# Performance work log

Measured on AMD Instinct MI355X. Metric: run time of the kernel, lower is better.

The kernel has to match this reference:

```python
import jax, jax.numpy as jnp
import numpy as np

# Hard-coded model hyperparams (RuntimeParams)
B, L, H, NH, FF, DEPTH = 256, 256, 128, 8, 512, 4
PEAK, NCAT, CVOC, KMAX, NNUM, NDIM, TSLOT = 500000, 8, 50001, 8, 4, 32, 256
SCALE = (H // NH) ** -0.5


def _ln(x, g, b):
    m = x.mean(-1, keepdims=True)
    v = ((x - m) ** 2).mean(-1, keepdims=True)
    return (x - m) / jnp.sqrt(v + 1e-5) * g + b


def _block(x, mask, p):
    ln1_g, ln1_b, qw, qb, ow, ob, w1, b1, w2, b2, ln2_g, ln2_b = p
    b, n, c = x.shape
    src = _ln(x, ln1_g, ln1_b)
    qkv = (src @ qw + qb).reshape(b, n, 3, NH, c // NH).transpose(2, 0, 3, 1, 4)
    q, k, v = qkv[0], qkv[1], qkv[2]  # [b, nh, n, dh]
    dots = jnp.einsum('bhid,bhjd->bhij', q, k) * SCALE
    dots = jnp.where(mask[:, None, None, :], dots, -jnp.inf)
    attn = jax.nn.softmax(dots, axis=-1)
    out = jnp.einsum('bhij,bhjd->bhid', attn, v).transpose(0, 2, 1, 3).reshape(b, n, c)
    x = x + out @ ow + ob
    h = _ln(x, ln2_g, ln2_b)
    h = jax.nn.gelu(h @ w1 + b1, approximate=False) @ w2 + b2
    return x + h


def _encode(cat_vals, cat_lens, num_arr, cat_tables, num_W):
    # Vectorized form of the per-sample _encode_fields python loop:
    # per categorical field: mean of embeddings over the ragged value list
    # per numeric field: bias-free linear projection; then mean over all fields.
    emb = cat_tables[jnp.arange(NCAT)[None, :, None], cat_vals]  # [B,F,K,H]
    pos = (jnp.arange(KMAX)[None, None, :] < cat_lens[:, :, None]).astype(emb.dtype)
    fc = (emb * pos[..., None]).sum(2) / cat_lens[:, :, None].astype(emb.dtype)  # [B,F,H]
    fn = jnp.einsum('bfd,fdh->bfh', num_arr, num_W)  # [B,Fn,H]
    return (fc.sum(1) + fn.sum(1)) / (NCAT + NNUM)  # mean over all fields


def setup_inputs() -> dict:
    key = jax.random.key(0)
    ks = iter(jax.random.split(key, 40))
    nk = lambda: next(ks)
    d = {}
    d['item_seq'] = jax.random.randint(nk(), (B, L), 0, PEAK + 5)
    d['action_seq'] = jax.random.randint(nk(), (B, L), 0, 5)
    d['time_diff'] = jax.random.randint(nk(), (B, L), 0, TSLOT)
    seq_lens = jax.random.randint(nk(), (B,), L // 2, L + 1)
    d['mask'] = jnp.arange(L)[None, :] < seq_lens[:, None]
    for pre in ('u', 'i'):
        vals = jax.random.randint(nk(), (B, NCAT, KMAX), 1, CVOC)
        lens = jax.random.randint(nk(), (B, NCAT), 1, KMAX + 1)
        vals = jnp.where(jnp.arange(KMAX)[None, None, :] < lens[:, :, None], vals, 0)
        d[pre + '_cat_vals'] = vals
        d[pre + '_cat_lens'] = lens
        d[pre + '_num'] = jax.random.normal(nk(), (B, NNUM, NDIM), dtype=jnp.float32)
    s = 0.02
    d['item_table'] = (jax.random.normal(nk(), (PEAK + 5, H), dtype=jnp.float32) * s).at[0].set(0.0)
    d['act_table'] = jax.random.normal(nk(), (5, H), dtype=jnp.float32) * s
    d['time_table'] = jax.random.normal(nk(), (TSLOT, H), dtype=jnp.float32) * s
    d['cat_tables'] = (jax.random.normal(nk(), (NCAT, CVOC, H), dtype=jnp.float32) * s).at[:, 0, :].set(0.0)
    d['num_W'] = jax.random.normal(nk(), (NNUM, NDIM, H), dtype=jnp.float32) * s
    d['global_token'] = jax.random.normal(nk(), (1, 1, H), dtype=jnp.float32)
    d['ln1_g'] = jnp.ones((DEPTH, H)); d['ln1_b'] = jnp.zeros((DEPTH, H))
    d['qkv_w'] = jax.random.normal(nk(), (DEPTH, H, 3 * H), dtype=jnp.float32) * s
    d['qkv_b'] = jnp.zeros((DEPTH, 3 * H))
    d['out_w'] = jax.random.normal(nk(), (DEPTH, H, H), dtype=jnp.float32) * s
    d['out_b'] = jnp.zeros((DEPTH, H))
    d['mlp_w1'] = jax.random.normal(nk(), (DEPTH, H, FF), dtype=jnp.float32) * s
    d['mlp_b1'] = jnp.zeros((DEPTH, FF))
    d['mlp_w2'] = jax.random.normal(nk(), (DEPTH, FF, H), dtype=jnp.float32) * s
    d['mlp_b2'] = jnp.zeros((DEPTH, H))
    d['ln2_g'] = jnp.ones((DEPTH, H)); d['ln2_b'] = jnp.zeros((DEPTH, H))
    d['bott_w'] = jax.random.normal(nk(), (H, H), dtype=jnp.float32) * s
    d['bott_b'] = jnp.zeros((H,))
    d['cls_w'] = jax.random.normal(nk(), (H, 1), dtype=jnp.float32) * s
    d['cls_b'] = jnp.zeros((1,))
    return d


def reference(item_seq, action_seq, time_diff, mask, u_cat_vals, u_cat_lens, u_num,
              i_cat_vals, i_cat_lens, i_num, item_table, act_table, time_table,
              cat_tables, num_W, global_token, ln1_g, ln1_b, qkv_w, qkv_b,
              out_w, out_b, mlp_w1, mlp_b1, mlp_w2, mlp_b2, ln2_g, ln2_b,
              bott_w, bott_b, cls_w, cls_b):
    b = item_seq.shape[0]
    seq_feat = item_table[item_seq] + act_table[action_seq] + time_table[time_diff]  # [B,L,H]
    u = _encode(u_cat_vals, u_cat_lens, u_num, cat_tables, num_W)[:, None, :]
    i = _encode(i_cat_vals, i_cat_lens, i_num, cat_tables, num_W)[:, None, :]
    cls = jnp.broadcast_to(global_token, (b, 1, H))
    x = jnp.concatenate([cls, u, i, seq_feat], axis=1)  # [B, 3+L, H]
    fmask = jnp.concatenate([jnp.ones((b, 3), dtype=bool), mask], axis=1)
    for dd in range(DEPTH):
        p = (ln1_g[dd], ln1_b[dd], qkv_w[dd], qkv_b[dd], out_w[dd], out_b[dd],
             mlp_w1[dd], mlp_b1[dd], mlp_w2[dd], mlp_b2[dd], ln2_g[dd], ln2_b[dd])
        x = _block(x, fmask, p)
    latent = x[:, 0, :]
    logits = (jax.nn.relu(latent @ bott_w + bott_b) @ cls_w + cls_b)[:, 0]
    embed = latent / jnp.maximum(jnp.linalg.norm(latent, axis=-1, keepdims=True), 1e-12)
    return logits, embed
```

## Files before the change

### kernel.cpp

```cpp
#include <hip/hip_runtime.h>
#include <cstdio>

#define BATCH 256
#define SEQL 256
#define NPOS 259
#define TTOK (BATCH*NPOS)
#define HD 128
#define NHEAD 8
#define FF 512
#define DEPTH 4
#define CVOC 50001

typedef unsigned short u16;
typedef unsigned int u32;
typedef __bf16 bf16x8 __attribute__((ext_vector_type(8)));
typedef float f32x4 __attribute__((ext_vector_type(4)));
typedef float f32x16 __attribute__((ext_vector_type(16)));

typedef const __attribute__((address_space(1))) u32 gas_u32;
typedef __attribute__((address_space(3))) u32 las_u32;
#define GLOAD16(gptr, lptr) \
  __builtin_amdgcn_global_load_lds((gas_u32*)(gptr), (las_u32*)(lptr), 16, 0, 0)

#define QSCALE 0.36067376022224085f

__device__ __forceinline__ u16 f2bf(float f) {
  u32 i = __float_as_uint(f);
  u32 r = (i + 0x7FFFu + ((i >> 16) & 1u)) >> 16;
  return (u16)r;
}
__device__ __forceinline__ float bf2f(u16 u) {
  return __uint_as_float(((u32)u) << 16);
}

__global__ void k_transpose_all(const float* __restrict__ qkv_w, const float* __restrict__ out_w,
                                const float* __restrict__ w1, const float* __restrict__ w2,
                                u16* __restrict__ wT) {
  int idx = blockIdx.x * 256 + threadIdx.x;
  const float* in; int K, N, local;
  if (idx < 196608)      { in = qkv_w; K = 128; N = 384; local = idx; }
  else if (idx < 262144) { in = out_w; K = 128; N = 128; local = idx - 196608; }
  else if (idx < 524288) { in = w1;    K = 128; N = 512; local = idx - 262144; }
  else if (idx < 786432) { in = w2;    K = 512; N = 128; local = idx - 524288; }
  else return;
  int k = local % K; int rem = local / K; int n = rem % N; int d = rem / N;
  wT[idx] = f2bf(in[(d * K + k) * N + n]);
}

__global__ __launch_bounds__(128)
void k_build(const int* __restrict__ item_seq, const int* __restrict__ act_seq,
             const int* __restrict__ tdiff,
             const int* __restrict__ ucv, const int* __restrict__ ucl, const float* __restrict__ unum,
             const int* __restrict__ icv, const int* __restrict__ icl, const float* __restrict__ inum,
             const float* __restrict__ item_t, const float* __restrict__ act_t,
             const float* __restrict__ time_t, const float* __restrict__ cat_t,
             const float* __restrict__ numW, const float* __restrict__ gtok,
             const float* __restrict__ g, const float* __restrict__ be,
             u16* __restrict__ x, u16* __restrict__ src) {
  int pos = blockIdx.x, b = blockIdx.y, h = threadIdx.x;
  float v;
  if (pos == 0) {
    v = gtok[h];
  } else if (pos <= 2) {
    const int* cv = (pos == 1) ? ucv : icv;
    const int* cl = (pos == 1) ? ucl : icl;
    const float* nm = (pos == 1) ? unum : inum;
    float acc = 0.f;
    for (int f = 0; f < 8; ++f) {
      float s = 0.f;
      for (int k = 0; k < 8; ++k) {
        int idx = cv[(b * 8 + f) * 8 + k];
        s += cat_t[((size_t)f * CVOC + idx) * HD + h];
      }
      acc += s / (float)cl[b * 8 + f];
    }
    for (int f = 0; f < 4; ++f)
      for (int d = 0; d < 32; ++d)
        acc += nm[(b * 4 + f) * 32 + d] * numW[(f * 32 + d) * HD + h];
    v = acc * (1.f / 12.f);
  } else {
    int l = pos - 3;
    v = item_t[(size_t)item_seq[b * SEQL + l] * HD + h]
      + act_t[(size_t)act_seq[b * SEQL + l] * HD + h]
      + time_t[(size_t)tdiff[b * SEQL + l] * HD + h];
  }
  size_t t = (size_t)b * NPOS + pos;
  x[t * HD + h] = f2bf(v);
  __shared__ float red[2][2];
  float s = v, s2 = v * v;
  #pragma unroll
  for (int o = 32; o; o >>= 1) { s += __shfl_xor(s, o); s2 += __shfl_xor(s2, o); }
  if ((h & 63) == 0) { red[h >> 6][0] = s; red[h >> 6][1] = s2; }
  __syncthreads();
  float S = red[0][0] + red[1][0], S2 = red[0][1] + red[1][1];
  float mean = S * (1.f / HD);
  float rstd = rsqrtf(S2 * (1.f / HD) - mean * mean + 1e-5f);
  src[t * HD + h] = f2bf((v - mean) * rstd * g[h] + be[h]);
}

template <int NCH, int ACT, bool QS>
__global__ __launch_bounds__(256)
void k_gemm_nres(const u16* __restrict__ X, const u16* __restrict__ WT,
                 const float* __restrict__ bias, u16* __restrict__ outp) {
  const int K = 128, N = NCH * 128;
  __shared__ __align__(16) u16 lA[4][32 * 32];
  __shared__ __align__(16) u16 lB[128 * 32];
  const int tid = threadIdx.x;
  const int wave = tid >> 6, lane = tid & 63;
  const int row0 = blockIdx.x * 32;
  const int wr = (wave >> 1) * 16, wc = (wave & 1) * 64;
  const int sr = lane >> 2;
  const int sc = ((lane & 3) ^ ((lane >> 3) & 3)) << 3;
  const int q = lane & 15;
  const int cg = lane >> 4;
  const int rdoff = ((cg ^ ((q >> 1) & 3)) << 3);
  GLOAD16(X + (size_t)(row0 + sr) * K + wave * 32 + sc, &lA[wave][0]);
  GLOAD16(X + (size_t)(row0 + 16 + sr) * K + wave * 32 + sc, &lA[wave][512]);
  const u16* gB0 = WT + (size_t)(wave * 16 + sr) * K + sc;
  const u16* gB1 = WT + (size_t)(64 + wave * 16 + sr) * K + sc;
  u16* lB0 = &lB[wave * 512];
  u16* lB1 = &lB[2048 + wave * 512];
  for (int nc = 0; nc < NCH; ++nc) {
    const size_t nbase = (size_t)nc * 128 * K;
    f32x4 acc[4] = {};
    for (int k0 = 0; k0 < K; k0 += 32) {
      __syncthreads();
      GLOAD16(gB0 + nbase + k0, lB0);
      GLOAD16(gB1 + nbase + k0, lB1);
      __syncthreads();
      const int kt = k0 >> 5;
      bf16x8 af = *(const bf16x8*)&lA[kt][(wr + q) * 32 + rdoff];
      bf16x8 bf[4];
      #pragma unroll
      for (int j = 0; j < 4; ++j)
        bf[j] = *(const bf16x8*)&lB[(wc + j * 16 + q) * 32 + rdoff];
      #pragma unroll
      for (int j = 0; j < 4; ++j)
        acc[j] = __builtin_amdgcn_mfma_f32_16x16x32_bf16(af, bf[j], acc[j], 0, 0, 0);
    }
    const int rg4 = cg * 4;
    const float scl = (QS && nc == 0) ? QSCALE : 1.f;
    #pragma unroll
    for (int j = 0; j < 4; ++j) {
      int col = nc * 128 + wc + j * 16 + q;
      float bv = bias[col];
      #pragma unroll
      for (int jj = 0; jj < 4; ++jj) {
        int row = row0 + wr + rg4 + jj;
        float v = acc[j][jj] + bv;
        if (ACT == 1) v = 0.5f * v * (1.f + erff(v * 0.70710678118654752f));
        if (QS) v *= scl;
        outp[(size_t)row * N + col] = f2bf(v);
      }
    }
  }
}

__global__ __launch_bounds__(256)
void k_gemm_ln(const u16* __restrict__ X, const u16* __restrict__ WT,
               const float* __restrict__ bias, u16* __restrict__ xio,
               const float* __restrict__ g, const float* __restrict__ be,
               u16* __restrict__ srcout, int K) {
  __shared__ __align__(16) u16 lA[32 * 32];
  __shared__ __align__(16) u16 lB[128 * 32];
  __shared__ float part[32][2][2];
  const int tid = threadIdx.x;
  const int wave = tid >> 6, lane = tid & 63;
  const int row0 = blockIdx.x * 32;
  const int wr = (wave >> 1) * 16, wc = (wave & 1) * 64;
  const int whalf = wave & 1;
  const int sr = lane >> 2;
  const int sc = ((lane & 3) ^ ((lane >> 3) & 3)) << 3;
  const u16* gA = X + (size_t)(row0 + (wave & 1) * 16 + sr) * K + sc;
  const u16* gB0 = WT + (size_t)(wave * 16 + sr) * K + sc;
  const u16* gB1 = WT + (size_t)(64 + wave * 16 + sr) * K + sc;
  u16* lA0 = &lA[(wave & 1) * 512];
  u16* lB0 = &lB[wave * 512];
  u16* lB1 = &lB[2048 + wave * 512];
  const int q = lane & 15;
  const int cg = lane >> 4;
  const int rdoff = ((cg ^ ((q >> 1) & 3)) << 3);
  f32x4 acc[4] = {};
  for (int k0 = 0; k0 < K; k0 += 32) {
    __syncthreads();
    if (wave < 2) GLOAD16(gA + k0, lA0);
    GLOAD16(gB0 + k0, lB0);
    GLOAD16(gB1 + k0, lB1);
    __syncthreads();
    bf16x8 af = *(const bf16x8*)&lA[(wr + q) * 32 + rdoff];
    bf16x8 bf[4];
    #pragma unroll
    for (int j = 0; j < 4; ++j)
      bf[j] = *(const bf16x8*)&lB[(wc + j * 16 + q) * 32 + rdoff];
    #pragma unroll
    for (int j = 0; j < 4; ++j)
      acc[j] = __builtin_amdgcn_mfma_f32_16x16x32_bf16(af, bf[j], acc[j], 0, 0, 0);
  }
  const int rg4 = cg * 4;
  float ps[4], ps2[4];
  #pragma unroll
  for (int jj = 0; jj < 4; ++jj) { ps[jj] = 0.f; ps2[jj] = 0.f; }
  #pragma unroll
  for (int j = 0; j < 4; ++j) {
    int col = wc + j * 16 + q;
    float bv = bias[col];
    #pragma unroll
    for (int jj = 0; jj < 4; ++jj) {
      int row = row0 + wr + rg4 + jj;
      float xv = bf2f(xio[(size_t)row * 128 + col]) + acc[j][jj] + bv;
      acc[j][jj] = xv;
      ps[jj] += xv;
      ps2[jj] += xv * xv;
    }
  }
  #pragma unroll
  for (int o = 1; o < 16; o <<= 1) {
    #pragma unroll
    for (int jj = 0; jj < 4; ++jj) {
      ps[jj]  += __shfl_xor(ps[jj], o);
      ps2[jj] += __shfl_xor(ps2[jj], o);
    }
  }
  if (q == 0) {
    #pragma unroll
    for (int jj = 0; jj < 4; ++jj) {
      int rl = wr + rg4 + jj;
      part[rl][whalf][0] = ps[jj];
      part[rl][whalf][1] = ps2[jj];
    }
  }
  __syncthreads();
  #pragma unroll
  for (int jj = 0; jj < 4; ++jj) {
    int rl = wr + rg4 + jj;
    float S  = part[rl][0][0] + part[rl][1][0];
    float S2 = part[rl][0][1] + part[rl][1][1];
    float mean = S * (1.f / 128.f);
    float rstd = rsqrtf(S2 * (1.f / 128.f) - mean * mean + 1e-5f);
    int row = row0 + rl;
    #pragma unroll
    for (int j = 0; j < 4; ++j) {
      int col = wc + j * 16 + q;
      float xv = acc[j][jj];
      xio[(size_t)row * 128 + col] = f2bf(xv);
      srcout[(size_t)row * 128 + col] = f2bf((xv - mean) * rstd * g[col] + be[col]);
    }
  }
}

#define VSTR2 296
__global__ __launch_bounds__(576)
void k_attn(const u16* __restrict__ qkv, const int* __restrict__ mask,
            u16* __restrict__ out) {
  int b = blockIdx.x, h = blockIdx.y;
  __shared__ __align__(16) u16 Klin[9 * 512];
  __shared__ __align__(16) u16 Vt[16 * VSTR2];
  __shared__ int part[4];
  const int tid = threadIdx.x;
  if (tid < 256) {
    int mv = (mask[b * SEQL + tid] != 0) ? 1 : 0;
    #pragma unroll
    for (int o = 32; o; o >>= 1) mv += __shfl_xor(mv, o);
    if ((tid & 63) == 0) part[tid >> 6] = mv;
  }
  {
    int r = tid >> 1, h2 = tid & 1;
    uint4 val = make_uint4(0, 0, 0, 0);
    if (r < NPOS)
      val = *(const uint4*)&qkv[((size_t)(b * NPOS + r)) * 384 + h * 16 + 128 + h2 * 8];
    *(uint4*)&Klin[(r >> 5) * 512 + h2 * 256 + (r & 31) * 8] = val;
  }
  {
    int r = tid >> 1, h2 = tid & 1;
    if (r < 288) {
      u16 tmp[8];
      if (r < NPOS) {
        *(uint4*)tmp = *(const uint4*)&qkv[((size_t)(b * NPOS + r)) * 384 + h * 16 + 256 + h2 * 8];
      } else {
        #pragma unroll
        for (int d = 0; d < 8; ++d) tmp[d] = 0;
      }
      #pragma unroll
      for (int d = 0; d < 8; ++d) Vt[(h2 * 8 + d) * VSTR2 + r] = tmp[d];
    }
  }
  __syncthreads();
  const int nvalid = part[0] + part[1] + part[2] + part[3] + 3;
  const int ktiles = (nvalid + 31) >> 5;
  const int wave = tid >> 6, lane = tid & 63;
  const int q5 = lane & 31, hi = lane >> 5;
  const f32x16 zf = {};
  const int qt = wave;
  int qrow = qt * 32 + q5;
  int qr = (qrow < NPOS) ? qrow : (NPOS - 1);
  bf16x8 qf = *(const bf16x8*)&qkv[((size_t)(b * NPOS + qr)) * 384 + h * 16 + hi * 8];
  float m = -1e30f, l = 0.f;
  f32x16 acc = {};
  for (int kt = 0; kt < ktiles; ++kt) {
    bf16x8 kf = *(const bf16x8*)&Klin[kt * 512 + lane * 8];
    __builtin_amdgcn_s_setprio(1);
    f32x16 s4 = __builtin_amdgcn_mfma_f32_32x32x16_bf16(kf, qf, zf, 0, 0, 0);
    __builtin_amdgcn_s_setprio(0);
    float p[16];
    float tmax = -1e30f;
    if ((kt + 1) * 32 <= nvalid) {
      #pragma unroll
      for (int r = 0; r < 16; ++r) { p[r] = s4[r]; tmax = fmaxf(tmax, s4[r]); }
    } else {
      #pragma unroll
      for (int r = 0; r < 16; ++r) {
        int kr = kt * 32 + (r & 3) + 8 * (r >> 2) + 4 * hi;
        float v = (kr < nvalid) ? s4[r] : -1e30f;
        p[r] = v;
        tmax = fmaxf(tmax, v);
      }
    }
    tmax = fmaxf(tmax, __shfl_xor(tmax, 32));
    bool defer = __all(tmax <= m + 8.f);
    float mnew = defer ? m : fmaxf(m, tmax);
    float fac = defer ? 1.f : exp2f(m - mnew);
    float tsum = 0.f;
    #pragma unroll
    for (int r = 0; r < 16; ++r) { p[r] = exp2f(p[r] - mnew); tsum += p[r]; }
    tsum += __shfl_xor(tsum, 32);
    l = l * fac + tsum;
    m = mnew;
    if (!defer) {
      #pragma unroll
      for (int r = 0; r < 8; ++r) acc[r] *= fac;
    }
    u32 w[8], xw[8];
    #pragma unroll
    for (int i = 0; i < 8; ++i)
      asm("v_cvt_pk_bf16_f32 %0, %1, %2" : "=v"(w[i]) : "v"(p[2 * i]), "v"(p[2 * i + 1]));
    #pragma unroll
    for (int i = 0; i < 8; ++i) xw[i] = (u32)__shfl_xor((int)w[i], 32);
    union { u32 u[4]; bf16x8 v; } f1, f2;
    if (hi) {
      f1.u[0] = xw[2]; f1.u[1] = xw[3]; f1.u[2] = w[2]; f1.u[3] = w[3];
      f2.u[0] = xw[6]; f2.u[1] = xw[7]; f2.u[2] = w[6]; f2.u[3] = w[7];
    } else {
      f1.u[0] = w[0]; f1.u[1] = w[1]; f1.u[2] = xw[0]; f1.u[3] = xw[1];
      f2.u[0] = w[4]; f2.u[1] = w[5]; f2.u[2] = xw[4]; f2.u[3] = xw[5];
    }
    bf16x8 vf0 = {}, vf1 = {};
    if (q5 < 16) {
      vf0 = *(const bf16x8*)&Vt[q5 * VSTR2 + kt * 32 + hi * 8];
      vf1 = *(const bf16x8*)&Vt[q5 * VSTR2 + kt * 32 + 16 + hi * 8];
    }
    __builtin_amdgcn_s_setprio(1);
    acc = __builtin_amdgcn_mfma_f32_32x32x16_bf16(vf0, f1.v, acc, 0, 0, 0);
    acc = __builtin_amdgcn_mfma_f32_32x32x16_bf16(vf1, f2.v, acc, 0, 0, 0);
    __builtin_amdgcn_s_setprio(0);
  }
  if (qrow < NPOS) {
    float linv = 1.f / l;
    u16* op = &out[((size_t)(b * NPOS + qrow)) * HD + h * 16];
    u32 w0 = (u32)f2bf(acc[0] * linv) | ((u32)f2bf(acc[1] * linv) << 16);
    u32 w1 = (u32)f2bf(acc[2] * linv) | ((u32)f2bf(acc[3] * linv) << 16);
    u32 w2 = (u32)f2bf(acc[4] * linv) | ((u32)f2bf(acc[5] * linv) << 16);
    u32 w3 = (u32)f2bf(acc[6] * linv) | ((u32)f2bf(acc[7] * linv) << 16);
    *(uint2*)&op[4 * hi] = make_uint2(w0, w1);
    *(uint2*)&op[8 + 4 * hi] = make_uint2(w2, w3);
  }
}

__global__ __launch_bounds__(128)
void k_head(const u16* __restrict__ x, const float* __restrict__ bw,
            const float* __restrict__ bb, const float* __restrict__ cw,
            const float* __restrict__ cb, float* __restrict__ dout) {
  int b = blockIdx.x, n = threadIdx.x;
  __shared__ float lat[HD];
  __shared__ float redp[2], redss[2];
  float lv = bf2f(x[((size_t)b * NPOS) * HD + n]);
  lat[n] = lv;
  __syncthreads();
  float t = 0.f;
  for (int k = 0; k < HD; ++k) t += lat[k] * bw[k * HD + n];
  t += bb[n];
  t = fmaxf(t, 0.f);
  float p = t * cw[n];
  float ss = lv * lv;
  #pragma unroll
  for (int o = 32; o; o >>= 1) { p += __shfl_xor(p, o); ss += __shfl_xor(ss, o); }
  if ((n & 63) == 0) { redp[n >> 6] = p; redss[n >> 6] = ss; }
  __syncthreads();
  float psum = redp[0] + redp[1];
  float ssum = redss[0] + redss[1];
  if (n == 0) dout[b] = psum + cb[0];
  float nrm = fmaxf(sqrtf(ssum), 1e-12f);
  dout[256 + (size_t)b * HD + n] = lv / nrm;
}

extern "C" void kernel_launch(void* const* d_in, const int* in_sizes, int n_in,
                              void* d_out, int out_size, void* d_ws, size_t ws_size,
                              hipStream_t stream) {
  const int* item_seq = (const int*)d_in[0];
  const int* action_seq = (const int*)d_in[1];
  const int* time_diff = (const int*)d_in[2];
  const int* mask = (const int*)d_in[3];
  const int* u_cv = (const int*)d_in[4];
  const int* u_cl = (const int*)d_in[5];
  const float* u_num = (const float*)d_in[6];
  const int* i_cv = (const int*)d_in[7];
  const int* i_cl = (const int*)d_in[8];
  const float* i_num = (const float*)d_in[9];
  const float* item_t = (const float*)d_in[10];
  const float* act_t = (const float*)d_in[11];
  const float* time_t = (const float*)d_in[12];
  const float* cat_t = (const float*)d_in[13];
  const float* num_W = (const float*)d_in[14];
  const float* gtok = (const float*)d_in[15];
  const float* ln1_g = (const float*)d_in[16];
  const float* ln1_b = (const float*)d_in[17];
  const float* qkv_w = (const float*)d_in[18];
  const float* qkv_b = (const float*)d_in[19];
  const float* out_w = (const float*)d_in[20];
  const float* out_b = (const float*)d_in[21];
  const float* w1 = (const float*)d_in[22];
  const float* b1 = (const float*)d_in[23];
  const float* w2 = (const float*)d_in[24];
  const float* b2 = (const float*)d_in[25];
  const float* ln2_g = (const float*)d_in[26];
  const float* ln2_b = (const float*)d_in[27];
  const float* bott_w = (const float*)d_in[28];
  const float* bott_b = (const float*)d_in[29];
  const float* cls_w = (const float*)d_in[30];
  const float* cls_b = (const float*)d_in[31];

  const size_t off_x   = 0;
  const size_t off_src = 16973824;
  const size_t off_big = 33947648;
  const size_t off_wT  = 101842944;
  const size_t need    = 103415808;
  if (ws_size < need) {
    fprintf(stderr, "kernel_launch: ws_size %zu < needed %zu\n", ws_size, need);
    return;
  }
  char* ws = (char*)d_ws;
  u16* x     = (u16*)(ws + off_x);
  u16* src   = (u16*)(ws + off_src);
  u16* big   = (u16*)(ws + off_big);
  u16* wT    = (u16*)(ws + off_wT);
  u16* qkvT  = wT;
  u16* outT  = wT + 196608;
  u16* w1T   = wT + 262144;
  u16* w2T   = wT + 524288;

  k_transpose_all<<<3072, 256, 0, stream>>>(qkv_w, out_w, w1, w2, wT);

  k_build<<<dim3(NPOS, BATCH), 128, 0, stream>>>(
      item_seq, action_seq, time_diff, u_cv, u_cl, u_num, i_cv, i_cl, i_num,
      item_t, act_t, time_t, cat_t, num_W, gtok, ln1_g, ln1_b, x, src);

  const int rt = TTOK / 32;
  for (int dd = 0; dd < DEPTH; ++dd) {
    k_gemm_nres<3, 0, true><<<rt, 256, 0, stream>>>(
        src, qkvT + dd * 49152, qkv_b + dd * 384, big);
    k_attn<<<dim3(BATCH, NHEAD), 576, 0, stream>>>(big, mask, src);
    k_gemm_ln<<<rt, 256, 0, stream>>>(
        src, outT + dd * 16384, out_b + dd * HD, x,
        ln2_g + dd * HD, ln2_b + dd * HD, src, 128);
    k_gemm_nres<4, 1, false><<<rt, 256, 0, stream>>>(
        src, w1T + dd * 65536, b1 + dd * FF, big);
    const float* ng = (dd < 3) ? (ln1_g + (dd + 1) * HD) : (ln1_g + dd * HD);
    const float* nb = (dd < 3) ? (ln1_b + (dd + 1) * HD) : (ln1_b + dd * HD);
    k_gemm_ln<<<rt, 256, 0, stream>>>(
        big, w2T + dd * 65536, b2 + dd * HD, x, ng, nb, src, 512);
  }

  k_head<<<BATCH, 128, 0, stream>>>(x, bott_w, bott_b, cls_w, cls_b, (float*)d_out);
}
```

Measured before the change: 686.2 us.

## Fuse residual-GEMM+LayerNorm with the following GEMM through shared memory

Introduces a templated kernel that runs the residual GEMM plus LayerNorm and keeps the normalized 32-row tile in swizzled LDS. It then immediately multiplies that tile by the next weight matrix: the MLP up-projection with GELU, or the next layer's QKV projection with the Q scale. This drops the LN output round trip through global memory and removes two launches per layer. The last layer uses a plain residual GEMM with no LN, since the final LN output was never consumed. It costs more LDS per block and keeps the same small 32-row tiles, so occupancy and weight reloading per block may limit the benefit. A separate QKV buffer enlarges the workspace.

```diff
diff --git a/kernel.cpp b/kernel.cpp
--- a/kernel.cpp
+++ b/kernel.cpp
@@ -156,19 +156,151 @@
   }
 }
 
+template <int K1, int NCH2, int ACT2, bool QS2>
 __global__ __launch_bounds__(256)
-void k_gemm_ln(const u16* __restrict__ X, const u16* __restrict__ WT,
-               const float* __restrict__ bias, u16* __restrict__ xio,
-               const float* __restrict__ g, const float* __restrict__ be,
-               u16* __restrict__ srcout, int K) {
+void k_fused(const u16* __restrict__ X, const u16* __restrict__ WT1,
+             const float* __restrict__ bias1, u16* __restrict__ xio,
+             const float* __restrict__ g, const float* __restrict__ be,
+             const u16* __restrict__ WT2, const float* __restrict__ bias2,
+             u16* __restrict__ out2) {
   __shared__ __align__(16) u16 lA[32 * 32];
   __shared__ __align__(16) u16 lB[128 * 32];
+  __shared__ __align__(16) u16 lnA[4][32 * 32];
   __shared__ float part[32][2][2];
   const int tid = threadIdx.x;
   const int wave = tid >> 6, lane = tid & 63;
   const int row0 = blockIdx.x * 32;
   const int wr = (wave >> 1) * 16, wc = (wave & 1) * 64;
   const int whalf = wave & 1;
+  const int sr = lane >> 2;
+  const int sc = ((lane & 3) ^ ((lane >> 3) & 3)) << 3;
+  const int q = lane & 15;
+  const int cg = lane >> 4;
+  const int rdoff = ((cg ^ ((q >> 1) & 3)) << 3);
+  const int rg4 = cg * 4;
+  {
+    const u16* gA = X + (size_t)(row0 + (wave & 1) * 16 + sr) * K1 + sc;
+    const u16* gB0 = WT1 + (size_t)(wave * 16 + sr) * K1 + sc;
+    const u16* gB1 = WT1 + (size_t)(64 + wave * 16 + sr) * K1 + sc;
+    u16* lA0 = &lA[(wave & 1) * 512];
+    u16* lB0 = &lB[wave * 512];
+    u16* lB1 = &lB[2048 + wave * 512];
+    f32x4 acc[4] = {};
+    for (int k0 = 0; k0 < K1; k0 += 32) {
+      __syncthreads();
+      if (wave < 2) GLOAD16(gA + k0, lA0);
+      GLOAD16(gB0 + k0, lB0);
+      GLOAD16(gB1 + k0, lB1);
+      __syncthreads();
+      bf16x8 af = *(const bf16x8*)&lA[(wr + q) * 32 + rdoff];
+      bf16x8 bf[4];
+      #pragma unroll
+      for (int j = 0; j < 4; ++j)
+        bf[j] = *(const bf16x8*)&lB[(wc + j * 16 + q) * 32 + rdoff];
+      #pragma unroll
+      for (int j = 0; j < 4; ++j)
+        acc[j] = __builtin_amdgcn_mfma_f32_16x16x32_bf16(af, bf[j], acc[j], 0, 0, 0);
+    }
+    float ps[4], ps2[4];
+    #pragma unroll
+    for (int jj = 0; jj < 4; ++jj) { ps[jj] = 0.f; ps2[jj] = 0.f; }
+    #pragma unroll
+    for (int j = 0; j < 4; ++j) {
+      int col = wc + j * 16 + q;
+      float bv = bias1[col];
+      #pragma unroll
+      for (int jj = 0; jj < 4; ++jj) {
+        int row = row0 + wr + rg4 + jj;
+        float xv = bf2f(xio[(size_t)row * 128 + col]) + acc[j][jj] + bv;
+        acc[j][jj] = xv;
+        ps[jj] += xv;
+        ps2[jj] += xv * xv;
+      }
+    }
+    #pragma unroll
+    for (int o = 1; o < 16; o <<= 1) {
+      #pragma unroll
+      for (int jj = 0; jj < 4; ++jj) {
+        ps[jj]  += __shfl_xor(ps[jj], o);
+        ps2[jj] += __shfl_xor(ps2[jj], o);
+      }
+    }
+    if (q == 0) {
+      #pragma unroll
+      for (int jj = 0; jj < 4; ++jj) {
+        int rl = wr + rg4 + jj;
+        part[rl][whalf][0] = ps[jj];
+        part[rl][whalf][1] = ps2[jj];
+      }
+    }
+    __syncthreads();
+    #pragma unroll
+    for (int jj = 0; jj < 4; ++jj) {
+      int rl = wr + rg4 + jj;
+      float S  = part[rl][0][0] + part[rl][1][0];
+      float S2 = part[rl][0][1] + part[rl][1][1];
+      float mean = S * (1.f / 128.f);
+      float rstd = rsqrtf(S2 * (1.f / 128.f) - mean * mean + 1e-5f);
+      int row = row0 + rl;
+      const int rsel = ((rl >> 1) & 3) << 3;
+      #pragma unroll
+      for (int j = 0; j < 4; ++j) {
+        int col = wc + j * 16 + q;
+        float xv = acc[j][jj];
+        xio[(size_t)row * 128 + col] = f2bf(xv);
+        u16 lnv = f2bf((xv - mean) * rstd * g[col] + be[col]);
+        lnA[col >> 5][rl * 32 + ((((col >> 3) & 3) << 3) ^ rsel) + (col & 7)] = lnv;
+      }
+    }
+  }
+  const u16* gB20 = WT2 + (size_t)(wave * 16 + sr) * 128 + sc;
+  const u16* gB21 = WT2 + (size_t)(64 + wave * 16 + sr) * 128 + sc;
+  u16* lB0 = &lB[wave * 512];
+  u16* lB1 = &lB[2048 + wave * 512];
+  for (int nc = 0; nc < NCH2; ++nc) {
+    const size_t nbase = (size_t)nc * 128 * 128;
+    f32x4 acc[4] = {};
+    for (int k0 = 0; k0 < 128; k0 += 32) {
+      __syncthreads();
+      GLOAD16(gB20 + nbase + k0, lB0);
+      GLOAD16(gB21 + nbase + k0, lB1);
+      __syncthreads();
+      const int kt = k0 >> 5;
+      bf16x8 af = *(const bf16x8*)&lnA[kt][(wr + q) * 32 + rdoff];
+      bf16x8 bf[4];
+      #pragma unroll
+      for (int j = 0; j < 4; ++j)
+        bf[j] = *(const bf16x8*)&lB[(wc + j * 16 + q) * 32 + rdoff];
+      #pragma unroll
+      for (int j = 0; j < 4; ++j)
+        acc[j] = __builtin_amdgcn_mfma_f32_16x16x32_bf16(af, bf[j], acc[j], 0, 0, 0);
+    }
+    const float scl = (QS2 && nc == 0) ? QSCALE : 1.f;
+    #pragma unroll
+    for (int j = 0; j < 4; ++j) {
+      int col = nc * 128 + wc + j * 16 + q;
+      float bv = bias2[col];
+      #pragma unroll
+      for (int jj = 0; jj < 4; ++jj) {
+        int row = row0 + wr + rg4 + jj;
+        float v = acc[j][jj] + bv;
+        if (ACT2 == 1) v = 0.5f * v * (1.f + erff(v * 0.70710678118654752f));
+        if (QS2) v *= scl;
+        out2[(size_t)row * (NCH2 * 128) + col] = f2bf(v);
+      }
+    }
+  }
+}
+
+__global__ __launch_bounds__(256)
+void k_gemm_res(const u16* __restrict__ X, const u16* __restrict__ WT,
+                const float* __restrict__ bias, u16* __restrict__ xio, int K) {
+  __shared__ __align__(16) u16 lA[32 * 32];
+  __shared__ __align__(16) u16 lB[128 * 32];
+  const int tid = threadIdx.x;
+  const int wave = tid >> 6, lane = tid & 63;
+  const int row0 = blockIdx.x * 32;
+  const int wr = (wave >> 1) * 16, wc = (wave & 1) * 64;
   const int sr = lane >> 2;
   const int sc = ((lane & 3) ^ ((lane >> 3) & 3)) << 3;
   const u16* gA = X + (size_t)(row0 + (wave & 1) * 16 + sr) * K + sc;
@@ -197,9 +329,6 @@
       acc[j] = __builtin_amdgcn_mfma_f32_16x16x32_bf16(af, bf[j], acc[j], 0, 0, 0);
   }
   const int rg4 = cg * 4;
-  float ps[4], ps2[4];
-  #pragma unroll
-  for (int jj = 0; jj < 4; ++jj) { ps[jj] = 0.f; ps2[jj] = 0.f; }
   #pragma unroll
   for (int j = 0; j < 4; ++j) {
     int col = wc + j * 16 + q;
@@ -208,42 +337,7 @@
     for (int jj = 0; jj < 4; ++jj) {
       int row = row0 + wr + rg4 + jj;
       float xv = bf2f(xio[(size_t)row * 128 + col]) + acc[j][jj] + bv;
-      acc[j][jj] = xv;
-      ps[jj] += xv;
-      ps2[jj] += xv * xv;
-    }
-  }
-  #pragma unroll
-  for (int o = 1; o < 16; o <<= 1) {
-    #pragma unroll
-    for (int jj = 0; jj < 4; ++jj) {
-      ps[jj]  += __shfl_xor(ps[jj], o);
-      ps2[jj] += __shfl_xor(ps2[jj], o);
-    }
-  }
-  if (q == 0) {
-    #pragma unroll
-    for (int jj = 0; jj < 4; ++jj) {
-      int rl = wr + rg4 + jj;
-      part[rl][whalf][0] = ps[jj];
-      part[rl][whalf][1] = ps2[jj];
-    }
-  }
-  __syncthreads();
-  #pragma unroll
-  for (int jj = 0; jj < 4; ++jj) {
-    int rl = wr + rg4 + jj;
-    float S  = part[rl][0][0] + part[rl][1][0];
-    float S2 = part[rl][0][1] + part[rl][1][1];
-    float mean = S * (1.f / 128.f);
-    float rstd = rsqrtf(S2 * (1.f / 128.f) - mean * mean + 1e-5f);
-    int row = row0 + rl;
-    #pragma unroll
-    for (int j = 0; j < 4; ++j) {
-      int col = wc + j * 16 + q;
-      float xv = acc[j][jj];
       xio[(size_t)row * 128 + col] = f2bf(xv);
-      srcout[(size_t)row * 128 + col] = f2bf((xv - mean) * rstd * g[col] + be[col]);
     }
   }
 }
@@ -428,24 +522,26 @@
   const float* cls_w = (const float*)d_in[30];
   const float* cls_b = (const float*)d_in[31];
 
-  const size_t off_x   = 0;
-  const size_t off_src = 16973824;
-  const size_t off_big = 33947648;
-  const size_t off_wT  = 101842944;
-  const size_t need    = 103415808;
+  const size_t off_x    = 0;
+  const size_t off_src  = 16973824;
+  const size_t off_h1   = 33947648;
+  const size_t off_qkv  = 101842944;
+  const size_t off_wT   = 152764416;
+  const size_t need     = 154337280;
   if (ws_size < need) {
     fprintf(stderr, "kernel_launch: ws_size %zu < needed %zu\n", ws_size, need);
     return;
   }
   char* ws = (char*)d_ws;
-  u16* x     = (u16*)(ws + off_x);
-  u16* src   = (u16*)(ws + off_src);
-  u16* big   = (u16*)(ws + off_big);
-  u16* wT    = (u16*)(ws + off_wT);
-  u16* qkvT  = wT;
-  u16* outT  = wT + 196608;
-  u16* w1T   = wT + 262144;
-  u16* w2T   = wT + 524288;
+  u16* x      = (u16*)(ws + off_x);
+  u16* src    = (u16*)(ws + off_src);
+  u16* h1buf  = (u16*)(ws + off_h1);
+  u16* qkvbuf = (u16*)(ws + off_qkv);
+  u16* wT     = (u16*)(ws + off_wT);
+  u16* qkvT   = wT;
+  u16* outT   = wT + 196608;
+  u16* w1T    = wT + 262144;
+  u16* w2T    = wT + 524288;
 
   k_transpose_all<<<3072, 256, 0, stream>>>(qkv_w, out_w, w1, w2, wT);
 
@@ -454,19 +550,22 @@
       item_t, act_t, time_t, cat_t, num_W, gtok, ln1_g, ln1_b, x, src);
 
   const int rt = TTOK / 32;
+  k_gemm_nres<3, 0, true><<<rt, 256, 0, stream>>>(src, qkvT, qkv_b, qkvbuf);
+
   for (int dd = 0; dd < DEPTH; ++dd) {
-    k_gemm_nres<3, 0, true><<<rt, 256, 0, stream>>>(
-        src, qkvT + dd * 49152, qkv_b + dd * 384, big);
-    k_attn<<<dim3(BATCH, NHEAD), 576, 0, stream>>>(big, mask, src);
-    k_gemm_ln<<<rt, 256, 0, stream>>>(
+    k_attn<<<dim3(BATCH, NHEAD), 576, 0, stream>>>(qkvbuf, mask, src);
+    k_fused<128, 4, 1, false><<<rt, 256, 0, stream>>>(
         src, outT + dd * 16384, out_b + dd * HD, x,
-        ln2_g + dd * HD, ln2_b + dd * HD, src, 128);
-    k_gemm_nres<4, 1, false><<<rt, 256, 0, stream>>>(
-        src, w1T + dd * 65536, b1 + dd * FF, big);
-    const float* ng = (dd < 3) ? (ln1_g + (dd + 1) * HD) : (ln1_g + dd * HD);
-    const float* nb = (dd < 3) ? (ln1_b + (dd + 1) * HD) : (ln1_b + dd * HD);
-    k_gemm_ln<<<rt, 256, 0, stream>>>(
-        big, w2T + dd * 65536, b2 + dd * HD, x, ng, nb, src, 512);
+        ln2_g + dd * HD, ln2_b + dd * HD,
+        w1T + dd * 65536, b1 + dd * FF, h1buf);
+    if (dd < 3) {
+      k_fused<512, 3, 0, true><<<rt, 256, 0, stream>>>(
+          h1buf, w2T + dd * 65536, b2 + dd * HD, x,
+          ln1_g + (dd + 1) * HD, ln1_b + (dd + 1) * HD,
+          qkvT + (dd + 1) * 49152, qkv_b + (dd + 1) * 384, qkvbuf);
+    } else {
+      k_gemm_res<<<rt, 256, 0, stream>>>(h1buf, w2T + dd * 65536, b2 + dd * HD, x, 512);
+    }
   }
 
   k_head<<<BATCH, 128, 0, stream>>>(x, bott_w, bott_b, cls_w, cls_b, (float*)d_out);
```

Measured after the change: 679.3 us. Within noise of the previous version (-1.0%).
